# Optimization experiments

Hardware: AMD Instinct MI355X
Metric: run time of the kernel (lower is better)

The kernel has to match this reference:

```python
import jax, jax.numpy as jnp
import numpy as np

jax.config.update("jax_enable_x64", True)  # original casts to double for Sinkhorn

SINKHORN_EPS = 0.003
SINKHORN_ITER = 50
MU = 0.25


def setup_inputs() -> dict:
    key = jax.random.key(0)
    k1, k2 = jax.random.split(key)
    x = jax.random.normal(k1, (4096, 4096), dtype=jnp.float32)        # [B, D]
    codebook = jax.random.normal(k2, (256, 4096), dtype=jnp.float32)  # [K, D]
    return {"x": x, "codebook": codebook}


def _sinkhorn_probs(d2term):
    # d2term: [B, K] squared distances (float32)
    B, K = d2term.shape
    max_d = jnp.max(d2term, axis=-1, keepdims=True)
    min_d = jnp.min(d2term, axis=-1, keepdims=True)
    mid_d = (max_d + min_d) / 2
    normed = ((d2term - mid_d) / (max_d - mid_d + 1e-8)).astype(jnp.float64)
    standard = jnp.exp(-normed / SINKHORN_EPS)
    standard = standard / standard.sum()  # sum over dim1 then dim0 == total sum

    def body(i, carry):
        s, n = carry
        s = s / s.sum(axis=0, keepdims=True)
        n = n / K
        s = s / s.sum(axis=1, keepdims=True)
        n = n / B
        return (s, n)

    standard, normed = jax.lax.fori_loop(0, SINKHORN_ITER, body, (standard, normed))
    # original returns d2term_normed * B as probs (d2term_standard is unused after loop)
    return normed * B


def reference(x, codebook):
    # squared euclidean distances: [B, K]
    d2term = (jnp.sum(x * x, axis=-1, keepdims=True)
              + jnp.sum(codebook * codebook, axis=-1)[None, :]
              - 2.0 * (x @ codebook.T))
    probs = _sinkhorn_probs(d2term)              # [B, K] float64
    indices = jnp.argmax(probs, axis=-1)         # [B] int
    quant_hard = codebook[indices]               # [B, D] gather
    # straight-through estimator
    quant = jax.lax.stop_gradient(quant_hard - x) + x
    codebook_loss = jnp.mean((quant_hard - jax.lax.stop_gradient(x)) ** 2, axis=-1)
    commitment_loss = jnp.mean((jax.lax.stop_gradient(quant_hard) - x) ** 2, axis=-1)
    loss = codebook_loss + MU * commitment_loss  # [B]
    return quant, indices, probs, loss
```

## Files before the change

### kernel.cpp

```cpp
#include <hip/hip_runtime.h>
#include <hip/hip_bf16.h>
#include <math.h>

#define D_DIM   4096
#define B_ROWS  4096
#define K_CODES 256
#define MARGIN  3.0
#define BK      256
#define NITER   (D_DIM / BK)
#define MT      16

#define IDX_OFF   (B_ROWS * D_DIM)
#define PROBS_OFF (IDX_OFF + B_ROWS)
#define LOSS_OFF  (PROBS_OFF + B_ROWS * K_CODES)

typedef __bf16 bf16x8 __attribute__((ext_vector_type(8)));
typedef float  f32x4  __attribute__((ext_vector_type(4)));


static __device__ inline unsigned short f2bf(float f) {
    __hip_bfloat16 h = __float2bfloat16(f);
    return *reinterpret_cast<unsigned short*>(&h);
}

__global__ __launch_bounds__(64) void prep_cb(const float* __restrict__ cb,
                                              unsigned short* __restrict__ cbsw,
                                              double* __restrict__ cc) {
    const int lane = threadIdx.x & 63;
    const int k = blockIdx.x;
    const float4* row4 = (const float4*)(cb + (size_t)k * D_DIM);
    double a0 = 0.0, a1 = 0.0, a2 = 0.0, a3 = 0.0;
#pragma unroll
    for (int i = 0; i < 16; ++i) {
        float4 v = row4[i * 64 + lane];
        a0 += (double)v.x * v.x; a1 += (double)v.y * v.y;
        a2 += (double)v.z * v.z; a3 += (double)v.w * v.w;
        ushort4 h;
        h.x = f2bf(v.x); h.y = f2bf(v.y); h.z = f2bf(v.z); h.w = f2bf(v.w);
        const int c = (i * 64 + lane) * 4;
        const size_t idx = (((size_t)(c >> 5) * 16 + (k >> 4)) * 64
                            + ((c >> 3) & 3) * 16 + (k & 15)) * 8 + (c & 7);
        *(ushort4*)&cbsw[idx] = h;
    }
    double s = (a0 + a1) + (a2 + a3);
    for (int off = 32; off; off >>= 1) s += __shfl_xor(s, off);
    if (lane == 0) cc[k] = s;
}

__global__ __launch_bounds__(512, 2) void vq(const float* __restrict__ x,
                                             const float* __restrict__ cb,
                                             const unsigned short* __restrict__ cbsw,
                                             const double* __restrict__ cc,
                                             float* __restrict__ out) {
    __shared__ unsigned short As[2][4096];
    __shared__ float d2s[MT][K_CODES];
    __shared__ float xxs[MT];
    const int t = threadIdx.x;
    const int lane = t & 63, w = t >> 6;
    const int m0 = blockIdx.x * MT;

    const int arow = t >> 5;
    const int ak = (t & 31) * 4;
    const float* ag = x + (size_t)(m0 + arow) * D_DIM + ak;
    const int aw0 = (ak >> 3) * 128 + arow * 8 + (ak & 7);
    const int aw1 = aw0 + 2048;
    const unsigned short* bbase = cbsw + ((size_t)w * 128 + lane) * 8;

    f32x4 acc0 = {0.f, 0.f, 0.f, 0.f}, acc1 = {0.f, 0.f, 0.f, 0.f};
    float sq = 0.f;

    float4 p0 = *(const float4*)(ag);
    float4 p1 = *(const float4*)(ag + 128);
    float4 c0 = *(const float4*)(ag + BK);
    float4 c1 = *(const float4*)(ag + BK + 128);
    bf16x8 b00 = *(const bf16x8*)(bbase);
    bf16x8 b01 = *(const bf16x8*)(bbase + 512);
    bf16x8 b10 = *(const bf16x8*)(bbase + 8192);
    bf16x8 b11 = *(const bf16x8*)(bbase + 8192 + 512);
    {
        ushort4 h0, h1;
        h0.x = f2bf(p0.x); h0.y = f2bf(p0.y); h0.z = f2bf(p0.z); h0.w = f2bf(p0.w);
        h1.x = f2bf(p1.x); h1.y = f2bf(p1.y); h1.z = f2bf(p1.z); h1.w = f2bf(p1.w);
        *(ushort4*)&As[0][aw0] = h0;
        *(ushort4*)&As[0][aw1] = h1;
        sq += p0.x*p0.x + p0.y*p0.y + p0.z*p0.z + p0.w*p0.w
            + p1.x*p1.x + p1.y*p1.y + p1.z*p1.z + p1.w*p1.w;
    }
    asm volatile("s_waitcnt lgkmcnt(0)" ::: "memory");
    __builtin_amdgcn_s_barrier();
    __builtin_amdgcn_sched_barrier(0);

    for (int it = 0; it < NITER; ++it) {
        const int p = it & 1;
        const unsigned short* Ap = &As[p][0];
        unsigned short* An = &As[p ^ 1][0];

        if (it + 1 < NITER) {
            ushort4 h0, h1;
            h0.x = f2bf(c0.x); h0.y = f2bf(c0.y); h0.z = f2bf(c0.z); h0.w = f2bf(c0.w);
            h1.x = f2bf(c1.x); h1.y = f2bf(c1.y); h1.z = f2bf(c1.z); h1.w = f2bf(c1.w);
            *(ushort4*)&An[aw0] = h0;
            *(ushort4*)&An[aw1] = h1;
            sq += c0.x*c0.x + c0.y*c0.y + c0.z*c0.z + c0.w*c0.w
                + c1.x*c1.x + c1.y*c1.y + c1.z*c1.z + c1.w*c1.w;
        }
        const int t2 = (it + 2 < NITER) ? (it + 2) * BK : 0;
        float4 n0 = *(const float4*)(ag + t2);
        float4 n1 = *(const float4*)(ag + t2 + 128);

        __builtin_amdgcn_s_setprio(1);
#pragma unroll
        for (int s = 0; s < 8; ++s) {
            bf16x8 af = *(const bf16x8*)&Ap[(s * 64 + lane) * 8];
            if (s & 1) {
                acc0 = __builtin_amdgcn_mfma_f32_16x16x32_bf16(af, b10, acc0, 0, 0, 0);
                acc1 = __builtin_amdgcn_mfma_f32_16x16x32_bf16(af, b11, acc1, 0, 0, 0);
            } else {
                acc0 = __builtin_amdgcn_mfma_f32_16x16x32_bf16(af, b00, acc0, 0, 0, 0);
                acc1 = __builtin_amdgcn_mfma_f32_16x16x32_bf16(af, b01, acc1, 0, 0, 0);
            }
            const int Ln = it * 8 + s + 2;
            const size_t bo = (size_t)((Ln < 128) ? Ln : 0) * 8192;
            if (s & 1) { b10 = *(const bf16x8*)(bbase + bo);
                         b11 = *(const bf16x8*)(bbase + bo + 512); }
            else       { b00 = *(const bf16x8*)(bbase + bo);
                         b01 = *(const bf16x8*)(bbase + bo + 512); }
        }
        __builtin_amdgcn_s_setprio(0);

        asm volatile("s_waitcnt lgkmcnt(0)" ::: "memory");
        __builtin_amdgcn_s_barrier();
        __builtin_amdgcn_sched_barrier(0);
        c0 = n0; c1 = n1;
    }

#pragma unroll
    for (int r = 0; r < 4; ++r) {
        const int orow = (lane >> 4) * 4 + r;
        d2s[orow][w * 32 + (lane & 15)]      = acc0[r];
        d2s[orow][w * 32 + 16 + (lane & 15)] = acc1[r];
    }
    sq += __shfl_xor(sq, 1); sq += __shfl_xor(sq, 2); sq += __shfl_xor(sq, 4);
    sq += __shfl_xor(sq, 8); sq += __shfl_xor(sq, 16);
    if ((t & 31) == 0) xxs[arow] = sq;
    __syncthreads();

#pragma unroll
    for (int rr = 0; rr < 2; ++rr) {
        const int r = w + 8 * rr;
        const int row = m0 + r;
        const double xx = (double)xxs[r];
        const float4 dv = ((const float4*)&d2s[r][0])[lane];
        double v[4];
        v[0] = xx + cc[4 * lane + 0] - 2.0 * (double)dv.x;
        v[1] = xx + cc[4 * lane + 1] - 2.0 * (double)dv.y;
        v[2] = xx + cc[4 * lane + 2] - 2.0 * (double)dv.z;
        v[3] = xx + cc[4 * lane + 3] - 2.0 * (double)dv.w;

        double mx = fmax(fmax(v[0], v[1]), fmax(v[2], v[3]));
        for (int off = 32; off; off >>= 1) mx = fmax(mx, __shfl_xor(mx, off));
        const double thr = mx - MARGIN;

        unsigned long long b[4];
#pragma unroll
        for (int j = 0; j < 4; ++j) b[j] = __ballot(v[j] >= thr);
        const int total = __popcll(b[0]) + __popcll(b[1]) + __popcll(b[2]) + __popcll(b[3]);

        int bestk = 0; double best;
        if (total == 1) {
            best = mx;
#pragma unroll
            for (int j = 0; j < 4; ++j)
                if (b[j]) bestk = 4 * (int)__builtin_ctzll(b[j]) + j;
        } else {
            const float4* xrow4 = (const float4*)(x + (size_t)row * D_DIM);
            int flags = 0;
#pragma unroll
            for (int j = 0; j < 4; ++j) if (v[j] >= thr) flags |= 1 << j;
            unsigned long long cand = __ballot(flags != 0);
            best = -1.0e300;
            while (cand) {
                const int lsrc = __builtin_ctzll(cand);
                cand &= cand - 1;
                const int f = __shfl(flags, lsrc);
                for (int j = 0; j < 4; ++j) {
                    if (!((f >> j) & 1)) continue;
                    const int k = 4 * lsrc + j;
                    const float4* crow4 = (const float4*)(cb + (size_t)k * D_DIM);
                    double a0 = 0.0, a1 = 0.0, a2 = 0.0, a3 = 0.0;
#pragma unroll
                    for (int i = 0; i < 16; ++i) {
                        float4 xa = xrow4[i * 64 + lane];
                        float4 ca = crow4[i * 64 + lane];
                        a0 += (double)xa.x * ca.x; a1 += (double)xa.y * ca.y;
                        a2 += (double)xa.z * ca.z; a3 += (double)xa.w * ca.w;
                    }
                    double s = (a0 + a1) + (a2 + a3);
                    for (int off = 32; off; off >>= 1) s += __shfl_xor(s, off);
                    const double d2e = xx + cc[k] - 2.0 * s;
                    if (d2e > best) { best = d2e; bestk = k; }
                }
            }
        }

        if (lane == 0) {
            out[IDX_OFF + row]  = (float)bestk;
            out[LOSS_OFF + row] = (float)(1.25 * best / (double)D_DIM);
        }
        float4 z = make_float4(0.f, 0.f, 0.f, 0.f);
        ((float4*)(out + PROBS_OFF + (size_t)row * K_CODES))[lane] = z;
        const float4* src = (const float4*)(cb + (size_t)bestk * D_DIM);
        float4* dst = (float4*)(out + (size_t)row * D_DIM);
#pragma unroll
        for (int i = 0; i < 16; ++i) dst[i * 64 + lane] = src[i * 64 + lane];
    }
}

extern "C" void kernel_launch(void* const* d_in, const int* in_sizes, int n_in,
                              void* d_out, int out_size, void* d_ws, size_t ws_size,
                              hipStream_t stream) {
    const float* x  = (const float*)d_in[0];
    const float* cb = (const float*)d_in[1];
    float* out = (float*)d_out;

    unsigned short* cbsw = (unsigned short*)d_ws;
    double*         cc   = (double*)((char*)d_ws + (size_t)K_CODES * D_DIM * sizeof(unsigned short));

    hipLaunchKernelGGL(prep_cb, dim3(256), dim3(64),  0, stream, cb, cbsw, cc);
    hipLaunchKernelGGL(vq,      dim3(256), dim3(512), 0, stream, x, cb, cbsw, cc, out);
}
```

Baseline: 158.8 us.

## Halve K-tile and prefetch whole codebook register banks per stage

```diff
diff --git a/kernel.cpp b/kernel.cpp
--- a/kernel.cpp
+++ b/kernel.cpp
@@ -6,7 +6,7 @@
 #define B_ROWS  4096
 #define K_CODES 256
 #define MARGIN  3.0
-#define BK      256
+#define BK      128
 #define NITER   (D_DIM / BK)
 #define MT      16
 
@@ -47,12 +47,36 @@
     if (lane == 0) cc[k] = s;
 }
 
+#define LOAD_BANK(bank, Lbase)                                              \
+    _Pragma("unroll")                                                       \
+    for (int s = 0; s < 4; ++s) {                                           \
+        bank[s][0] = *(const bf16x8*)(bbase + ((size_t)(Lbase) + s) * 8192);        \
+        bank[s][1] = *(const bf16x8*)(bbase + ((size_t)(Lbase) + s) * 8192 + 512);  \
+    }
+
+#define MFMA_TILE(Ap, bank)                                                 \
+    _Pragma("unroll")                                                       \
+    for (int s = 0; s < 4; ++s) {                                           \
+        bf16x8 af = *(const bf16x8*)&Ap[(s * 64 + lane) * 8];               \
+        acc0 = __builtin_amdgcn_mfma_f32_16x16x32_bf16(af, bank[s][0], acc0, 0, 0, 0); \
+        acc1 = __builtin_amdgcn_mfma_f32_16x16x32_bf16(af, bank[s][1], acc1, 0, 0, 0); \
+    }
+
+#define STAGE_A(buf, v)                                                     \
+    {                                                                       \
+        ushort4 hh;                                                         \
+        hh.x = f2bf((v).x); hh.y = f2bf((v).y);                             \
+        hh.z = f2bf((v).z); hh.w = f2bf((v).w);                             \
+        *(ushort4*)&buf[aw] = hh;                                           \
+        sq += (v).x*(v).x + (v).y*(v).y + (v).z*(v).z + (v).w*(v).w;        \
+    }
+
 __global__ __launch_bounds__(512, 2) void vq(const float* __restrict__ x,
                                              const float* __restrict__ cb,
                                              const unsigned short* __restrict__ cbsw,
                                              const double* __restrict__ cc,
                                              float* __restrict__ out) {
-    __shared__ unsigned short As[2][4096];
+    __shared__ unsigned short As[2][2048];
     __shared__ float d2s[MT][K_CODES];
     __shared__ float xxs[MT];
     const int t = threadIdx.x;
@@ -62,76 +86,52 @@
     const int arow = t >> 5;
     const int ak = (t & 31) * 4;
     const float* ag = x + (size_t)(m0 + arow) * D_DIM + ak;
-    const int aw0 = (ak >> 3) * 128 + arow * 8 + (ak & 7);
-    const int aw1 = aw0 + 2048;
+    const int aw = (ak >> 3) * 128 + arow * 8 + (ak & 7);
     const unsigned short* bbase = cbsw + ((size_t)w * 128 + lane) * 8;
 
     f32x4 acc0 = {0.f, 0.f, 0.f, 0.f}, acc1 = {0.f, 0.f, 0.f, 0.f};
     float sq = 0.f;
 
+    bf16x8 bA[4][2], bB[4][2];
+
+    LOAD_BANK(bA, 0)
     float4 p0 = *(const float4*)(ag);
-    float4 p1 = *(const float4*)(ag + 128);
-    float4 c0 = *(const float4*)(ag + BK);
-    float4 c1 = *(const float4*)(ag + BK + 128);
-    bf16x8 b00 = *(const bf16x8*)(bbase);
-    bf16x8 b01 = *(const bf16x8*)(bbase + 512);
-    bf16x8 b10 = *(const bf16x8*)(bbase + 8192);
-    bf16x8 b11 = *(const bf16x8*)(bbase + 8192 + 512);
-    {
-        ushort4 h0, h1;
-        h0.x = f2bf(p0.x); h0.y = f2bf(p0.y); h0.z = f2bf(p0.z); h0.w = f2bf(p0.w);
-        h1.x = f2bf(p1.x); h1.y = f2bf(p1.y); h1.z = f2bf(p1.z); h1.w = f2bf(p1.w);
-        *(ushort4*)&As[0][aw0] = h0;
-        *(ushort4*)&As[0][aw1] = h1;
-        sq += p0.x*p0.x + p0.y*p0.y + p0.z*p0.z + p0.w*p0.w
-            + p1.x*p1.x + p1.y*p1.y + p1.z*p1.z + p1.w*p1.w;
-    }
+    float4 cA = *(const float4*)(ag + BK);
+    float4 cB;
+    STAGE_A(As[0], p0)
     asm volatile("s_waitcnt lgkmcnt(0)" ::: "memory");
     __builtin_amdgcn_s_barrier();
     __builtin_amdgcn_sched_barrier(0);
 
-    for (int it = 0; it < NITER; ++it) {
-        const int p = it & 1;
-        const unsigned short* Ap = &As[p][0];
-        unsigned short* An = &As[p ^ 1][0];
-
-        if (it + 1 < NITER) {
-            ushort4 h0, h1;
-            h0.x = f2bf(c0.x); h0.y = f2bf(c0.y); h0.z = f2bf(c0.z); h0.w = f2bf(c0.w);
-            h1.x = f2bf(c1.x); h1.y = f2bf(c1.y); h1.z = f2bf(c1.z); h1.w = f2bf(c1.w);
-            *(ushort4*)&An[aw0] = h0;
-            *(ushort4*)&An[aw1] = h1;
-            sq += c0.x*c0.x + c0.y*c0.y + c0.z*c0.z + c0.w*c0.w
-                + c1.x*c1.x + c1.y*c1.y + c1.z*c1.z + c1.w*c1.w;
-        }
-        const int t2 = (it + 2 < NITER) ? (it + 2) * BK : 0;
-        float4 n0 = *(const float4*)(ag + t2);
-        float4 n1 = *(const float4*)(ag + t2 + 128);
-
+    for (int itp = 0; itp < 16; ++itp) {
+        STAGE_A(As[1], cA)
+        {
+            const int nt = (2 * itp + 2 < NITER) ? (2 * itp + 2) : 0;
+            cB = *(const float4*)(ag + (size_t)nt * BK);
+        }
+        LOAD_BANK(bB, (2 * itp + 1) * 4)
         __builtin_amdgcn_s_setprio(1);
-#pragma unroll
-        for (int s = 0; s < 8; ++s) {
-            bf16x8 af = *(const bf16x8*)&Ap[(s * 64 + lane) * 8];
-            if (s & 1) {
-                acc0 = __builtin_amdgcn_mfma_f32_16x16x32_bf16(af, b10, acc0, 0, 0, 0);
-                acc1 = __builtin_amdgcn_mfma_f32_16x16x32_bf16(af, b11, acc1, 0, 0, 0);
-            } else {
-                acc0 = __builtin_amdgcn_mfma_f32_16x16x32_bf16(af, b00, acc0, 0, 0, 0);
-                acc1 = __builtin_amdgcn_mfma_f32_16x16x32_bf16(af, b01, acc1, 0, 0, 0);
-            }
-            const int Ln = it * 8 + s + 2;
-            const size_t bo = (size_t)((Ln < 128) ? Ln : 0) * 8192;
-            if (s & 1) { b10 = *(const bf16x8*)(bbase + bo);
-                         b11 = *(const bf16x8*)(bbase + bo + 512); }
-            else       { b00 = *(const bf16x8*)(bbase + bo);
-                         b01 = *(const bf16x8*)(bbase + bo + 512); }
-        }
+        MFMA_TILE(As[0], bA)
         __builtin_amdgcn_s_setprio(0);
-
         asm volatile("s_waitcnt lgkmcnt(0)" ::: "memory");
         __builtin_amdgcn_s_barrier();
         __builtin_amdgcn_sched_barrier(0);
-        c0 = n0; c1 = n1;
+
+        if (itp < 15) STAGE_A(As[0], cB)
+        {
+            const int nt = (2 * itp + 3 < NITER) ? (2 * itp + 3) : 0;
+            cA = *(const float4*)(ag + (size_t)nt * BK);
+        }
+        {
+            const int Lb = (2 * itp + 2 < NITER) ? (2 * itp + 2) * 4 : 0;
+            LOAD_BANK(bA, Lb)
+        }
+        __builtin_amdgcn_s_setprio(1);
+        MFMA_TILE(As[1], bB)
+        __builtin_amdgcn_s_setprio(0);
+        asm volatile("s_waitcnt lgkmcnt(0)" ::: "memory");
+        __builtin_amdgcn_s_barrier();
+        __builtin_amdgcn_sched_barrier(0);
     }
 
 #pragma unroll
```

Result: no change. 157.4 us (-0.9%).
